# Performance work log

Measured on AMD Instinct MI355X. Metric: run time of the kernel, lower is better.

The kernel has to match this reference:

```python
import jax, jax.numpy as jnp
import numpy as np

B, S, DIM = 1, 2048, 4096
N_HEADS, N_KV_HEADS, HEAD_DIM = 32, 8, 128
REPEATS = N_HEADS // N_KV_HEADS
SLIDING_WINDOW = 2048
ROPE_THETA = 10000.0
NEG_INF = -1e9


def _rope_freqs(seqlen, head_dim):
    inv_freq = 1.0 / (ROPE_THETA ** (np.arange(0, head_dim, 2, dtype=np.float32) / head_dim))
    angles = np.arange(seqlen, dtype=np.float32)[:, None] * inv_freq[None, :]  # (S, D/2)
    return jnp.asarray(np.cos(angles)), jnp.asarray(np.sin(angles))


def _sliding_window_mask(seqlen, window):
    i = np.arange(seqlen)[:, None]
    j = np.arange(seqlen)[None, :]
    ok = (j <= i) & (i - j < window)
    return jnp.asarray(np.where(ok, 0.0, NEG_INF).astype(np.float32))


def setup_inputs() -> dict:
    key = jax.random.key(0)
    ks = jax.random.split(key, 5)
    x = jax.random.normal(ks[0], (B, S, DIM), dtype=jnp.float32)
    wq = jax.random.normal(ks[1], (N_HEADS * HEAD_DIM, DIM), dtype=jnp.float32) * 0.02
    wk = jax.random.normal(ks[2], (N_KV_HEADS * HEAD_DIM, DIM), dtype=jnp.float32) * 0.02
    wv = jax.random.normal(ks[3], (N_KV_HEADS * HEAD_DIM, DIM), dtype=jnp.float32) * 0.02
    wo = jax.random.normal(ks[4], (N_HEADS * HEAD_DIM, DIM), dtype=jnp.float32).T * 0.02
    wo = jnp.asarray(wo)  # (DIM, N_HEADS*HEAD_DIM), torch Linear weight layout (out,in)
    freqs_cos, freqs_sin = _rope_freqs(S, HEAD_DIM)
    mask = _sliding_window_mask(S, SLIDING_WINDOW)
    positions = jnp.arange(S, dtype=jnp.int64 if jax.config.jax_enable_x64 else jnp.int32)
    return {"x": x, "freqs_cos": freqs_cos, "freqs_sin": freqs_sin, "mask": mask,
            "positions": positions, "wq": wq, "wk": wk, "wv": wv, "wo": wo}


def _apply_rope(t, cos, sin):
    # t: (B, S, H, D); cos/sin: (S, D/2) broadcast as (1, S, 1, D/2)
    tr = t.reshape(*t.shape[:-1], -1, 2)
    re, im = tr[..., 0], tr[..., 1]
    c = cos[None, :, None, :]
    s = sin[None, :, None, :]
    out_re = re * c - im * s
    out_im = re * s + im * c
    return jnp.stack([out_re, out_im], axis=-1).reshape(t.shape)


def reference(x, freqs_cos, freqs_sin, mask, positions, wq, wk, wv, wo):
    bsz, seqlen, _ = x.shape
    xq = (x @ wq.T).reshape(bsz, seqlen, N_HEADS, HEAD_DIM)
    xk = (x @ wk.T).reshape(bsz, seqlen, N_KV_HEADS, HEAD_DIM)
    xv = (x @ wv.T).reshape(bsz, seqlen, N_KV_HEADS, HEAD_DIM)
    xq = _apply_rope(xq, freqs_cos, freqs_sin)
    xk = _apply_rope(xk, freqs_cos, freqs_sin)
    # prefill path (positions.shape[0] > 1): GQA repeat of current K/V
    key = jnp.repeat(xk, REPEATS, axis=2)   # (B, S, N_HEADS, D)
    value = jnp.repeat(xv, REPEATS, axis=2)
    scale = HEAD_DIM ** (-0.5)
    scores = jnp.einsum('bqhd,bkhd->bhqk', xq, key) * scale
    scores = scores + mask[None, None, :, :]
    probs = jax.nn.softmax(scores.astype(jnp.float32), axis=-1).astype(xq.dtype)
    out = jnp.einsum('bhqk,bkhd->bqhd', probs, value)
    out = out.reshape(bsz, seqlen, N_HEADS * HEAD_DIM)
    return out @ wo.T
```

## Files before the change

kernel.cpp:

```cpp
#include <hip/hip_runtime.h>

typedef __attribute__((ext_vector_type(4))) float f32x4;
typedef __attribute__((ext_vector_type(16))) float f32x16;
typedef __attribute__((ext_vector_type(8))) short bf16x8;
typedef __attribute__((ext_vector_type(4))) unsigned short u16x4;
typedef __attribute__((ext_vector_type(2))) unsigned short u16x2;
typedef __attribute__((ext_vector_type(4))) unsigned int u32x4;

#define SEQ 2048
#define DMODEL 4096

__device__ __forceinline__ unsigned short f2bf(float f) {
  unsigned int u = __float_as_uint(f);
  u += 0x7FFFu + ((u >> 16) & 1u);
  return (unsigned short)(u >> 16);
}

__device__ __forceinline__ void gload_lds16(const unsigned short* g, unsigned short* l) {
  __builtin_amdgcn_global_load_lds(
      (const __attribute__((address_space(1))) unsigned int*)g,
      (__attribute__((address_space(3))) unsigned int*)l, 16, 0, 0);
}

__device__ __forceinline__ unsigned int cvt_pk_bf16(float lo, float hi) {
  unsigned int r;
  asm("v_cvt_pk_bf16_f32 %0, %1, %2" : "=v"(r) : "v"(lo), "v"(hi));
  return r;
}

__global__ __launch_bounds__(256) void cvt_bf16(const float* __restrict__ in,
                                                unsigned short* __restrict__ out, int n4) {
  int i = blockIdx.x * 256 + threadIdx.x;
  if (i >= n4) return;
  f32x4 v = *(const f32x4*)(in + (size_t)i * 4);
  u16x4 o;
  o[0] = f2bf(v[0]); o[1] = f2bf(v[1]); o[2] = f2bf(v[2]); o[3] = f2bf(v[3]);
  *(u16x4*)(out + (size_t)i * 4) = o;
}

__global__ __launch_bounds__(256) void gemm_bt(const unsigned short* __restrict__ A,
                                               const unsigned short* __restrict__ B,
                                               float* __restrict__ C, int N) {
  __shared__ unsigned short As[128 * 64];
  __shared__ unsigned short Bs[128 * 64];
  const int K = 4096;
  const int bm = blockIdx.x, bn = blockIdx.y;
  const int t = threadIdx.x;
  const int lane = t & 63, w = t >> 6;
  const int wm = w >> 1, wn = w & 1;
  const int g = lane >> 4, q = lane & 15;

  const int srow = t >> 3;
  const int slb = (t & 7) ^ (srow & 7);
  const unsigned short* gA = A + (size_t)(bm * 128 + srow) * K + slb * 8;
  const unsigned short* gB = B + (size_t)(bn * 128 + srow) * K + slb * 8;
  unsigned short* lA = As + t * 8;
  unsigned short* lB = Bs + t * 8;

  f32x4 acc[4][4];
  for (int i = 0; i < 4; ++i)
    for (int j = 0; j < 4; ++j)
      for (int r = 0; r < 4; ++r) acc[i][j][r] = 0.f;

  for (int k0 = 0; k0 < K; k0 += 64) {
#pragma unroll
    for (int i = 0; i < 4; ++i) {
      gload_lds16(gA + (size_t)i * 32 * K + k0, lA + i * 2048);
      gload_lds16(gB + (size_t)i * 32 * K + k0, lB + i * 2048);
    }
    __syncthreads();
#pragma unroll
    for (int kk = 0; kk < 2; ++kk) {
      bf16x8 af[4], bfr[4];
#pragma unroll
      for (int i = 0; i < 4; ++i) {
        const int ra = wm * 64 + i * 16 + q;
        af[i] = *(const bf16x8*)&As[ra * 64 + (((kk * 4 + g) ^ (ra & 7)) * 8)];
        const int rb = wn * 64 + i * 16 + q;
        bfr[i] = *(const bf16x8*)&Bs[rb * 64 + (((kk * 4 + g) ^ (rb & 7)) * 8)];
      }
#pragma unroll
      for (int i = 0; i < 4; ++i)
#pragma unroll
        for (int j = 0; j < 4; ++j)
          acc[i][j] = __builtin_amdgcn_mfma_f32_16x16x32_bf16(af[i], bfr[j], acc[i][j], 0, 0, 0);
    }
    __syncthreads();
  }

  const int crow0 = bm * 128 + wm * 64 + g * 4;
  const int ccol0 = bn * 128 + wn * 64 + q;
#pragma unroll
  for (int i = 0; i < 4; ++i)
#pragma unroll
    for (int j = 0; j < 4; ++j) {
      float* cp = C + (size_t)(crow0 + i * 16) * N + ccol0 + j * 16;
#pragma unroll
      for (int r = 0; r < 4; ++r) cp[(size_t)r * N] = acc[i][j][r];
    }
}

__global__ __launch_bounds__(256) void rope_relayout(const float* __restrict__ X,
                                                     const float* __restrict__ cosT,
                                                     const float* __restrict__ sinT,
                                                     unsigned short* __restrict__ out,
                                                     int nheads, int ld) {
  int idx = blockIdx.x * 256 + threadIdx.x;
  int m = idx & 63;
  int h = (idx >> 6) % nheads;
  int s = idx / (nheads * 64);
  if (s >= SEQ) return;
  const float* xp = X + (size_t)s * ld + h * 128 + 2 * m;
  float re = xp[0], im = xp[1];
  float c = cosT[s * 64 + m], sn = sinT[s * 64 + m];
  u16x2 o;
  o[0] = f2bf(re * c - im * sn);
  o[1] = f2bf(re * sn + im * c);
  *(u16x2*)(out + ((size_t)h * SEQ + s) * 128 + 2 * m) = o;
}

__global__ __launch_bounds__(256) void v_transpose(const float* __restrict__ Vf,
                                                   unsigned short* __restrict__ VT) {
  __shared__ float tile[32][33];
  int s0 = blockIdx.x * 32, d0 = blockIdx.y * 32;
  int tx = threadIdx.x & 31, ty = threadIdx.x >> 5;
  for (int i = ty; i < 32; i += 8)
    tile[i][tx] = Vf[(size_t)(s0 + i) * 1024 + d0 + tx];
  __syncthreads();
  for (int i = ty; i < 32; i += 8)
    VT[(size_t)(d0 + i) * SEQ + s0 + tx] = f2bf(tile[tx][i]);
}

__global__ __launch_bounds__(256, 2) void attn_kernel(const unsigned short* __restrict__ Qh,
                                                      const unsigned short* __restrict__ Kh,
                                                      const unsigned short* __restrict__ VT,
                                                      unsigned short* __restrict__ Out) {
  const int x = blockIdx.x;
  const int h = (x & 7) * 4 + ((x >> 3) & 3);
  const int chunk = 15 - (x >> 5);
  const int kvh = h >> 2;
  const int t = threadIdx.x, w = t >> 6, lane = t & 63;
  const int ln = lane & 31, hi = lane >> 5;
  const int q0 = chunk * 128 + w * 32;

  const unsigned short* Qp = Qh + ((size_t)h * SEQ + q0 + ln) * 128 + hi * 8;
  const unsigned short* Kp = Kh + ((size_t)kvh * SEQ + ln) * 128 + hi * 8;
  const unsigned short* Vp = VT + ((size_t)(kvh * 128 + ln)) * SEQ + hi * 8;

  bf16x8 qf[8];
#pragma unroll
  for (int ds = 0; ds < 8; ++ds) qf[ds] = *(const bf16x8*)(Qp + ds * 16);

  f32x16 acc[4];
#pragma unroll
  for (int dt = 0; dt < 4; ++dt)
#pragma unroll
    for (int r = 0; r < 16; ++r) acc[dt][r] = 0.f;

  float m_run = -1e30f, l_run = 0.f;
  const float SCL = 0.08838834764831845f * 1.44269504088896f;

  for (int k0 = 0; k0 <= q0; k0 += 32) {
    bf16x8 vf[4][2];
#pragma unroll
    for (int dt = 0; dt < 4; ++dt)
#pragma unroll
      for (int ks = 0; ks < 2; ++ks)
        vf[dt][ks] = *(const bf16x8*)(Vp + (size_t)dt * 32 * SEQ + k0 + ks * 16);

    bf16x8 kf[8];
    const unsigned short* kp = Kp + (size_t)k0 * 128;
#pragma unroll
    for (int ds = 0; ds < 8; ++ds) kf[ds] = *(const bf16x8*)(kp + ds * 16);
    f32x16 s0, s1;
#pragma unroll
    for (int r = 0; r < 16; ++r) { s0[r] = 0.f; s1[r] = 0.f; }
#pragma unroll
    for (int ds = 0; ds < 4; ++ds) {
      s0 = __builtin_amdgcn_mfma_f32_32x32x16_bf16(kf[ds], qf[ds], s0, 0, 0, 0);
      s1 = __builtin_amdgcn_mfma_f32_32x32x16_bf16(kf[ds + 4], qf[ds + 4], s1, 0, 0, 0);
    }

    float sv[16];
#pragma unroll
    for (int r = 0; r < 16; ++r) {
      int kg = k0 + (r & 3) + 8 * (r >> 2) + 4 * hi;
      float vv = s0[r] + s1[r];
      sv[r] = (kg <= q0 + ln) ? vv : -1e30f;
    }
    float mx01 = fmaxf(sv[0], sv[1]), mx23 = fmaxf(sv[2], sv[3]);
    float mx45 = fmaxf(sv[4], sv[5]), mx67 = fmaxf(sv[6], sv[7]);
    float mx89 = fmaxf(sv[8], sv[9]), mxab = fmaxf(sv[10], sv[11]);
    float mxcd = fmaxf(sv[12], sv[13]), mxef = fmaxf(sv[14], sv[15]);
    float pm = fmaxf(fmaxf(fmaxf(mx01, mx23), fmaxf(mx45, mx67)),
                     fmaxf(fmaxf(mx89, mxab), fmaxf(mxcd, mxef)));
    pm = fmaxf(pm, __shfl_xor(pm, 32, 64));

    if (__any((pm - m_run) * SCL > 8.f)) {
      float m_new = fmaxf(m_run, pm);
      float corr = exp2f((m_run - m_new) * SCL);
      l_run *= corr;
#pragma unroll
      for (int r = 0; r < 16; ++r) {
        float cf = __shfl(corr, (r & 3) + 8 * (r >> 2) + 4 * hi, 64);
        acc[0][r] *= cf; acc[1][r] *= cf; acc[2][r] *= cf; acc[3][r] *= cf;
      }
      m_run = m_new;
    }

    float pv[16];
#pragma unroll
    for (int r = 0; r < 16; ++r) pv[r] = exp2f((sv[r] - m_run) * SCL);
    float a0 = (pv[0] + pv[1]) + (pv[2] + pv[3]);
    float a1 = (pv[4] + pv[5]) + (pv[6] + pv[7]);
    float a2 = (pv[8] + pv[9]) + (pv[10] + pv[11]);
    float a3 = (pv[12] + pv[13]) + (pv[14] + pv[15]);
    float ps = (a0 + a1) + (a2 + a3);
    ps += __shfl_xor(ps, 32, 64);
    l_run += ps;

    bf16x8 pa[2];
#pragma unroll
    for (int ks = 0; ks < 2; ++ks) {
      unsigned int X0 = cvt_pk_bf16(pv[8 * ks + 0], pv[8 * ks + 1]);
      unsigned int X1 = cvt_pk_bf16(pv[8 * ks + 2], pv[8 * ks + 3]);
      unsigned int Y0 = cvt_pk_bf16(pv[8 * ks + 4], pv[8 * ks + 5]);
      unsigned int Y1 = cvt_pk_bf16(pv[8 * ks + 6], pv[8 * ks + 7]);
      unsigned int sX0 = (unsigned int)__shfl_xor((int)X0, 32, 64);
      unsigned int sX1 = (unsigned int)__shfl_xor((int)X1, 32, 64);
      unsigned int sY0 = (unsigned int)__shfl_xor((int)Y0, 32, 64);
      unsigned int sY1 = (unsigned int)__shfl_xor((int)Y1, 32, 64);
      u32x4 pw;
      pw[0] = hi ? sY0 : X0;
      pw[1] = hi ? sY1 : X1;
      pw[2] = hi ? Y0 : sX0;
      pw[3] = hi ? Y1 : sX1;
      pa[ks] = __builtin_bit_cast(bf16x8, pw);
    }

#pragma unroll
    for (int dt = 0; dt < 4; ++dt) {
      acc[dt] = __builtin_amdgcn_mfma_f32_32x32x16_bf16(pa[0], vf[dt][0], acc[dt], 0, 0, 0);
      acc[dt] = __builtin_amdgcn_mfma_f32_32x32x16_bf16(pa[1], vf[dt][1], acc[dt], 0, 0, 0);
    }
  }

  float inv = 1.0f / l_run;
#pragma unroll
  for (int r = 0; r < 16; ++r) {
    float il = __shfl(inv, (r & 3) + 8 * (r >> 2) + 4 * hi, 64);
    int qg = q0 + (r & 3) + 8 * (r >> 2) + 4 * hi;
    unsigned short* op = Out + (size_t)qg * DMODEL + h * 128 + ln;
#pragma unroll
    for (int dt = 0; dt < 4; ++dt) op[dt * 32] = f2bf(acc[dt][r] * il);
  }
}

extern "C" void kernel_launch(void* const* d_in, const int* in_sizes, int n_in,
                              void* d_out, int out_size, void* d_ws, size_t ws_size,
                              hipStream_t stream) {
  (void)in_sizes; (void)n_in; (void)out_size; (void)ws_size;
  const float* x  = (const float*)d_in[0];
  const float* fc = (const float*)d_in[1];
  const float* fs = (const float*)d_in[2];
  const float* wq = (const float*)d_in[5];
  const float* wk = (const float*)d_in[6];
  const float* wv = (const float*)d_in[7];
  const float* wo = (const float*)d_in[8];
  float* out = (float*)d_out;

  char* ws = (char*)d_ws;
  const size_t MB = 1ull << 20;
  unsigned short* xb    = (unsigned short*)(ws + 0);
  unsigned short* wqb   = (unsigned short*)(ws + 16 * MB);
  unsigned short* wkb   = (unsigned short*)(ws + 48 * MB);
  unsigned short* wvb   = (unsigned short*)(ws + 56 * MB);
  float*          Qf    = (float*)(ws + 64 * MB);
  float*          Kf    = (float*)(ws + 96 * MB);
  float*          Vf    = (float*)(ws + 104 * MB);
  unsigned short* Qhb   = (unsigned short*)(ws + 112 * MB);
  unsigned short* Khb   = (unsigned short*)(ws + 128 * MB);
  unsigned short* VTb   = (unsigned short*)(ws + 132 * MB);
  unsigned short* attnb = (unsigned short*)(ws + 64 * MB);
  unsigned short* wob   = (unsigned short*)(ws + 16 * MB);

  cvt_bf16<<<8192, 256, 0, stream>>>(x, xb, 8388608 / 4);
  cvt_bf16<<<16384, 256, 0, stream>>>(wq, wqb, 16777216 / 4);
  cvt_bf16<<<4096, 256, 0, stream>>>(wk, wkb, 4194304 / 4);
  cvt_bf16<<<4096, 256, 0, stream>>>(wv, wvb, 4194304 / 4);

  gemm_bt<<<dim3(16, 32), 256, 0, stream>>>(xb, wqb, Qf, 4096);
  gemm_bt<<<dim3(16, 8), 256, 0, stream>>>(xb, wkb, Kf, 1024);
  gemm_bt<<<dim3(16, 8), 256, 0, stream>>>(xb, wvb, Vf, 1024);

  cvt_bf16<<<16384, 256, 0, stream>>>(wo, wob, 16777216 / 4);

  rope_relayout<<<16384, 256, 0, stream>>>(Qf, fc, fs, Qhb, 32, 4096);
  rope_relayout<<<4096, 256, 0, stream>>>(Kf, fc, fs, Khb, 8, 1024);
  v_transpose<<<dim3(64, 32), 256, 0, stream>>>(Vf, VTb);

  attn_kernel<<<512, 256, 0, stream>>>(Qhb, Khb, VTb, attnb);

  gemm_bt<<<dim3(16, 32), 256, 0, stream>>>(attnb, wob, out, 4096);
}
```

Before: 689.2 us.

## Balance causal attention work with paired tiles and split-K merge; fuse small launches

The attention kernel now pairs a short and a long causal query tile (p and 63-p) in each 128-thread block. The two waves split the key range of each tile and merge their partial softmax states through shared memory. This evens out per-block work and doubles the block count, so the causal triangle's load imbalance and tail shrink. It also merges the four fp32-to-bf16 conversions into one launch and the K and V projection GEMMs into one launch to cut launch overhead and raise occupancy. The cost is extra LDS traffic, barriers and a rescaling merge step per tile.

```diff
diff --git a/kernel.cpp b/kernel.cpp
--- a/kernel.cpp
+++ b/kernel.cpp
@@ -26,6 +26,24 @@
   unsigned int r;
   asm("v_cvt_pk_bf16_f32 %0, %1, %2" : "=v"(r) : "v"(lo), "v"(hi));
   return r;
+}
+
+__global__ __launch_bounds__(256) void cvt_bf16_multi(
+    const float* __restrict__ s0, unsigned short* __restrict__ d0, int n0,
+    const float* __restrict__ s1, unsigned short* __restrict__ d1, int n1,
+    const float* __restrict__ s2, unsigned short* __restrict__ d2, int n2,
+    const float* __restrict__ s3, unsigned short* __restrict__ d3, int n3) {
+  int i = blockIdx.x * 256 + threadIdx.x;
+  const float* s; unsigned short* d; int j = i;
+  if (j < n0) { s = s0; d = d0; }
+  else if ((j -= n0) < n1) { s = s1; d = d1; }
+  else if ((j -= n1) < n2) { s = s2; d = d2; }
+  else if ((j -= n2) < n3) { s = s3; d = d3; }
+  else return;
+  f32x4 v = *(const f32x4*)(s + (size_t)j * 4);
+  u16x4 o;
+  o[0] = f2bf(v[0]); o[1] = f2bf(v[1]); o[2] = f2bf(v[2]); o[3] = f2bf(v[3]);
+  *(u16x4*)(d + (size_t)j * 4) = o;
 }
 
 __global__ __launch_bounds__(256) void cvt_bf16(const float* __restrict__ in,
@@ -38,13 +56,13 @@
   *(u16x4*)(out + (size_t)i * 4) = o;
 }
 
-__global__ __launch_bounds__(256) void gemm_bt(const unsigned short* __restrict__ A,
-                                               const unsigned short* __restrict__ B,
-                                               float* __restrict__ C, int N) {
+__device__ __forceinline__ void gemm_bt_body(const unsigned short* __restrict__ A,
+                                             const unsigned short* __restrict__ B,
+                                             float* __restrict__ C, int N,
+                                             int bm, int bn) {
   __shared__ unsigned short As[128 * 64];
   __shared__ unsigned short Bs[128 * 64];
   const int K = 4096;
-  const int bm = blockIdx.x, bn = blockIdx.y;
   const int t = threadIdx.x;
   const int lane = t & 63, w = t >> 6;
   const int wm = w >> 1, wn = w & 1;
@@ -98,6 +116,22 @@
 #pragma unroll
       for (int r = 0; r < 4; ++r) cp[(size_t)r * N] = acc[i][j][r];
     }
+}
+
+__global__ __launch_bounds__(256) void gemm_bt(const unsigned short* __restrict__ A,
+                                               const unsigned short* __restrict__ B,
+                                               float* __restrict__ C, int N) {
+  gemm_bt_body(A, B, C, N, blockIdx.x, blockIdx.y);
+}
+
+__global__ __launch_bounds__(256) void gemm_bt_kv(const unsigned short* __restrict__ A,
+                                                  const unsigned short* __restrict__ BK,
+                                                  const unsigned short* __restrict__ BV,
+                                                  float* __restrict__ CK,
+                                                  float* __restrict__ CV) {
+  const int bn = blockIdx.y;
+  if (bn < 8) gemm_bt_body(A, BK, CK, 1024, blockIdx.x, bn);
+  else        gemm_bt_body(A, BV, CV, 1024, blockIdx.x, bn - 8);
 }
 
 __global__ __launch_bounds__(256) void rope_relayout(const float* __restrict__ X,
@@ -131,128 +165,171 @@
     VT[(size_t)(d0 + i) * SEQ + s0 + tx] = f2bf(tile[tx][i]);
 }
 
-__global__ __launch_bounds__(256, 2) void attn_kernel(const unsigned short* __restrict__ Qh,
+__global__ __launch_bounds__(128, 4) void attn_kernel(const unsigned short* __restrict__ Qh,
                                                       const unsigned short* __restrict__ Kh,
                                                       const unsigned short* __restrict__ VT,
                                                       unsigned short* __restrict__ Out) {
-  const int x = blockIdx.x;
-  const int h = (x & 7) * 4 + ((x >> 3) & 3);
-  const int chunk = 15 - (x >> 5);
+  __shared__ float mbuf[2][32];
+  __shared__ float lbuf[2][32];
+  __shared__ float abuf[64 * 64];
+
+  const int b = blockIdx.x;
+  const int h = (b & 7) * 4 + ((b >> 3) & 3);
+  const int p = b >> 5;
   const int kvh = h >> 2;
   const int t = threadIdx.x, w = t >> 6, lane = t & 63;
   const int ln = lane & 31, hi = lane >> 5;
-  const int q0 = chunk * 128 + w * 32;
-
-  const unsigned short* Qp = Qh + ((size_t)h * SEQ + q0 + ln) * 128 + hi * 8;
+
   const unsigned short* Kp = Kh + ((size_t)kvh * SEQ + ln) * 128 + hi * 8;
   const unsigned short* Vp = VT + ((size_t)(kvh * 128 + ln)) * SEQ + hi * 8;
-
-  bf16x8 qf[8];
-#pragma unroll
-  for (int ds = 0; ds < 8; ++ds) qf[ds] = *(const bf16x8*)(Qp + ds * 16);
-
-  f32x16 acc[4];
-#pragma unroll
-  for (int dt = 0; dt < 4; ++dt)
-#pragma unroll
-    for (int r = 0; r < 16; ++r) acc[dt][r] = 0.f;
-
-  float m_run = -1e30f, l_run = 0.f;
   const float SCL = 0.08838834764831845f * 1.44269504088896f;
 
-  for (int k0 = 0; k0 <= q0; k0 += 32) {
-    bf16x8 vf[4][2];
+  const int nA = p + 1, nB = 64 - p;
+  const int loA = (nA + 1) >> 1, loB = (nB + 1) >> 1;
+
+  for (int s = 0; s < 2; ++s) {
+    const int tile = (s == 0) ? p : 63 - p;
+    const int q0 = tile * 32;
+    int kbeg, kend;
+    if (s == 0) { kbeg = w ? loA : 0;  kend = w ? nA : loA; }
+    else        { kbeg = w ? 0 : loB;  kend = w ? loB : nB; }
+
+    const unsigned short* Qp = Qh + ((size_t)h * SEQ + q0 + ln) * 128 + hi * 8;
+    bf16x8 qf[8];
+#pragma unroll
+    for (int ds = 0; ds < 8; ++ds) qf[ds] = *(const bf16x8*)(Qp + ds * 16);
+
+    f32x16 acc[4];
 #pragma unroll
     for (int dt = 0; dt < 4; ++dt)
 #pragma unroll
-      for (int ks = 0; ks < 2; ++ks)
-        vf[dt][ks] = *(const bf16x8*)(Vp + (size_t)dt * 32 * SEQ + k0 + ks * 16);
-
-    bf16x8 kf[8];
-    const unsigned short* kp = Kp + (size_t)k0 * 128;
-#pragma unroll
-    for (int ds = 0; ds < 8; ++ds) kf[ds] = *(const bf16x8*)(kp + ds * 16);
-    f32x16 s0, s1;
-#pragma unroll
-    for (int r = 0; r < 16; ++r) { s0[r] = 0.f; s1[r] = 0.f; }
-#pragma unroll
-    for (int ds = 0; ds < 4; ++ds) {
-      s0 = __builtin_amdgcn_mfma_f32_32x32x16_bf16(kf[ds], qf[ds], s0, 0, 0, 0);
-      s1 = __builtin_amdgcn_mfma_f32_32x32x16_bf16(kf[ds + 4], qf[ds + 4], s1, 0, 0, 0);
-    }
-
-    float sv[16];
-#pragma unroll
-    for (int r = 0; r < 16; ++r) {
-      int kg = k0 + (r & 3) + 8 * (r >> 2) + 4 * hi;
-      float vv = s0[r] + s1[r];
-      sv[r] = (kg <= q0 + ln) ? vv : -1e30f;
-    }
-    float mx01 = fmaxf(sv[0], sv[1]), mx23 = fmaxf(sv[2], sv[3]);
-    float mx45 = fmaxf(sv[4], sv[5]), mx67 = fmaxf(sv[6], sv[7]);
-    float mx89 = fmaxf(sv[8], sv[9]), mxab = fmaxf(sv[10], sv[11]);
-    float mxcd = fmaxf(sv[12], sv[13]), mxef = fmaxf(sv[14], sv[15]);
-    float pm = fmaxf(fmaxf(fmaxf(mx01, mx23), fmaxf(mx45, mx67)),
-                     fmaxf(fmaxf(mx89, mxab), fmaxf(mxcd, mxef)));
-    pm = fmaxf(pm, __shfl_xor(pm, 32, 64));
-
-    if (__any((pm - m_run) * SCL > 8.f)) {
-      float m_new = fmaxf(m_run, pm);
-      float corr = exp2f((m_run - m_new) * SCL);
-      l_run *= corr;
+      for (int r = 0; r < 16; ++r) acc[dt][r] = 0.f;
+    float m_run = -1e30f, l_run = 0.f;
+
+    for (int kc = kbeg; kc < kend; ++kc) {
+      const int k0 = kc * 32;
+      bf16x8 vf[4][2];
+#pragma unroll
+      for (int dt = 0; dt < 4; ++dt)
+#pragma unroll
+        for (int ks = 0; ks < 2; ++ks)
+          vf[dt][ks] = *(const bf16x8*)(Vp + (size_t)dt * 32 * SEQ + k0 + ks * 16);
+
+      bf16x8 kf[8];
+      const unsigned short* kp = Kp + (size_t)k0 * 128;
+#pragma unroll
+      for (int ds = 0; ds < 8; ++ds) kf[ds] = *(const bf16x8*)(kp + ds * 16);
+      f32x16 s0v, s1v;
+#pragma unroll
+      for (int r = 0; r < 16; ++r) { s0v[r] = 0.f; s1v[r] = 0.f; }
+#pragma unroll
+      for (int ds = 0; ds < 4; ++ds) {
+        s0v = __builtin_amdgcn_mfma_f32_32x32x16_bf16(kf[ds], qf[ds], s0v, 0, 0, 0);
+        s1v = __builtin_amdgcn_mfma_f32_32x32x16_bf16(kf[ds + 4], qf[ds + 4], s1v, 0, 0, 0);
+      }
+
+      float sv[16];
 #pragma unroll
       for (int r = 0; r < 16; ++r) {
-        float cf = __shfl(corr, (r & 3) + 8 * (r >> 2) + 4 * hi, 64);
-        acc[0][r] *= cf; acc[1][r] *= cf; acc[2][r] *= cf; acc[3][r] *= cf;
-      }
-      m_run = m_new;
-    }
-
-    float pv[16];
-#pragma unroll
-    for (int r = 0; r < 16; ++r) pv[r] = exp2f((sv[r] - m_run) * SCL);
-    float a0 = (pv[0] + pv[1]) + (pv[2] + pv[3]);
-    float a1 = (pv[4] + pv[5]) + (pv[6] + pv[7]);
-    float a2 = (pv[8] + pv[9]) + (pv[10] + pv[11]);
-    float a3 = (pv[12] + pv[13]) + (pv[14] + pv[15]);
-    float ps = (a0 + a1) + (a2 + a3);
-    ps += __shfl_xor(ps, 32, 64);
-    l_run += ps;
-
-    bf16x8 pa[2];
-#pragma unroll
-    for (int ks = 0; ks < 2; ++ks) {
-      unsigned int X0 = cvt_pk_bf16(pv[8 * ks + 0], pv[8 * ks + 1]);
-      unsigned int X1 = cvt_pk_bf16(pv[8 * ks + 2], pv[8 * ks + 3]);
-      unsigned int Y0 = cvt_pk_bf16(pv[8 * ks + 4], pv[8 * ks + 5]);
-      unsigned int Y1 = cvt_pk_bf16(pv[8 * ks + 6], pv[8 * ks + 7]);
-      unsigned int sX0 = (unsigned int)__shfl_xor((int)X0, 32, 64);
-      unsigned int sX1 = (unsigned int)__shfl_xor((int)X1, 32, 64);
-      unsigned int sY0 = (unsigned int)__shfl_xor((int)Y0, 32, 64);
-      unsigned int sY1 = (unsigned int)__shfl_xor((int)Y1, 32, 64);
-      u32x4 pw;
-      pw[0] = hi ? sY0 : X0;
-      pw[1] = hi ? sY1 : X1;
-      pw[2] = hi ? Y0 : sX0;
-      pw[3] = hi ? Y1 : sX1;
-      pa[ks] = __builtin_bit_cast(bf16x8, pw);
-    }
-
-#pragma unroll
-    for (int dt = 0; dt < 4; ++dt) {
-      acc[dt] = __builtin_amdgcn_mfma_f32_32x32x16_bf16(pa[0], vf[dt][0], acc[dt], 0, 0, 0);
-      acc[dt] = __builtin_amdgcn_mfma_f32_32x32x16_bf16(pa[1], vf[dt][1], acc[dt], 0, 0, 0);
-    }
-  }
-
-  float inv = 1.0f / l_run;
-#pragma unroll
-  for (int r = 0; r < 16; ++r) {
-    float il = __shfl(inv, (r & 3) + 8 * (r >> 2) + 4 * hi, 64);
-    int qg = q0 + (r & 3) + 8 * (r >> 2) + 4 * hi;
-    unsigned short* op = Out + (size_t)qg * DMODEL + h * 128 + ln;
-#pragma unroll
-    for (int dt = 0; dt < 4; ++dt) op[dt * 32] = f2bf(acc[dt][r] * il);
+        int kg = k0 + (r & 3) + 8 * (r >> 2) + 4 * hi;
+        float vv = s0v[r] + s1v[r];
+        sv[r] = (kg <= q0 + ln) ? vv : -1e30f;
+      }
+      float mx01 = fmaxf(sv[0], sv[1]), mx23 = fmaxf(sv[2], sv[3]);
+      float mx45 = fmaxf(sv[4], sv[5]), mx67 = fmaxf(sv[6], sv[7]);
+      float mx89 = fmaxf(sv[8], sv[9]), mxab = fmaxf(sv[10], sv[11]);
+      float mxcd = fmaxf(sv[12], sv[13]), mxef = fmaxf(sv[14], sv[15]);
+      float pm = fmaxf(fmaxf(fmaxf(mx01, mx23), fmaxf(mx45, mx67)),
+                       fmaxf(fmaxf(mx89, mxab), fmaxf(mxcd, mxef)));
+      pm = fmaxf(pm, __shfl_xor(pm, 32, 64));
+
+      if (__any((pm - m_run) * SCL > 8.f)) {
+        float m_new = fmaxf(m_run, pm);
+        float corr = exp2f((m_run - m_new) * SCL);
+        l_run *= corr;
+#pragma unroll
+        for (int r = 0; r < 16; ++r) {
+          float cf = __shfl(corr, (r & 3) + 8 * (r >> 2) + 4 * hi, 64);
+          acc[0][r] *= cf; acc[1][r] *= cf; acc[2][r] *= cf; acc[3][r] *= cf;
+        }
+        m_run = m_new;
+      }
+
+      float pv[16];
+#pragma unroll
+      for (int r = 0; r < 16; ++r) pv[r] = exp2f((sv[r] - m_run) * SCL);
+      float a0 = (pv[0] + pv[1]) + (pv[2] + pv[3]);
+      float a1 = (pv[4] + pv[5]) + (pv[6] + pv[7]);
+      float a2 = (pv[8] + pv[9]) + (pv[10] + pv[11]);
+      float a3 = (pv[12] + pv[13]) + (pv[14] + pv[15]);
+      float ps = (a0 + a1) + (a2 + a3);
+      ps += __shfl_xor(ps, 32, 64);
+      l_run += ps;
+
+      bf16x8 pa[2];
+#pragma unroll
+      for (int ks = 0; ks < 2; ++ks) {
+        unsigned int X0 = cvt_pk_bf16(pv[8 * ks + 0], pv[8 * ks + 1]);
+        unsigned int X1 = cvt_pk_bf16(pv[8 * ks + 2], pv[8 * ks + 3]);
+        unsigned int Y0 = cvt_pk_bf16(pv[8 * ks + 4], pv[8 * ks + 5]);
+        unsigned int Y1 = cvt_pk_bf16(pv[8 * ks + 6], pv[8 * ks + 7]);
+        unsigned int sX0 = (unsigned int)__shfl_xor((int)X0, 32, 64);
+        unsigned int sX1 = (unsigned int)__shfl_xor((int)X1, 32, 64);
+        unsigned int sY0 = (unsigned int)__shfl_xor((int)Y0, 32, 64);
+        unsigned int sY1 = (unsigned int)__shfl_xor((int)Y1, 32, 64);
+        u32x4 pw;
+        pw[0] = hi ? sY0 : X0;
+        pw[1] = hi ? sY1 : X1;
+        pw[2] = hi ? Y0 : sX0;
+        pw[3] = hi ? Y1 : sX1;
+        pa[ks] = __builtin_bit_cast(bf16x8, pw);
+      }
+
+#pragma unroll
+      for (int dt = 0; dt < 4; ++dt) {
+        acc[dt] = __builtin_amdgcn_mfma_f32_32x32x16_bf16(pa[0], vf[dt][0], acc[dt], 0, 0, 0);
+        acc[dt] = __builtin_amdgcn_mfma_f32_32x32x16_bf16(pa[1], vf[dt][1], acc[dt], 0, 0, 0);
+      }
+    }
+
+    if (hi == 0) { mbuf[w][ln] = m_run; lbuf[w][ln] = l_run; }
+    __syncthreads();
+
+    const int wW = (s == 0) ? 1 : 0;
+    if (w == wW) {
+#pragma unroll
+      for (int r = 0; r < 16; ++r) {
+        const int row = (r & 3) + 8 * (r >> 2) + 4 * hi;
+        float m0 = mbuf[0][row], m1 = mbuf[1][row];
+        float ms = fmaxf(m0, m1);
+        float fown = exp2f(((w ? m1 : m0) - ms) * SCL);
+#pragma unroll
+        for (int dt = 0; dt < 4; ++dt)
+          abuf[(dt * 16 + r) * 64 + lane] = acc[dt][r] * fown;
+      }
+    }
+    __syncthreads();
+    if (w != wW) {
+#pragma unroll
+      for (int r = 0; r < 16; ++r) {
+        const int row = (r & 3) + 8 * (r >> 2) + 4 * hi;
+        float m0 = mbuf[0][row], m1 = mbuf[1][row];
+        float ms = fmaxf(m0, m1);
+        float f0 = exp2f((m0 - ms) * SCL);
+        float f1 = exp2f((m1 - ms) * SCL);
+        float ls = lbuf[0][row] * f0 + lbuf[1][row] * f1;
+        float inv = 1.0f / ls;
+        float fown = w ? f1 : f0;
+        const int qg = q0 + row;
+        unsigned short* op = Out + (size_t)qg * DMODEL + h * 128 + ln;
+#pragma unroll
+        for (int dt = 0; dt < 4; ++dt) {
+          float val = (acc[dt][r] * fown + abuf[(dt * 16 + r) * 64 + lane]) * inv;
+          op[dt * 32] = f2bf(val);
+        }
+      }
+    }
+    __syncthreads();
   }
 }
 
@@ -284,14 +361,13 @@
   unsigned short* attnb = (unsigned short*)(ws + 64 * MB);
   unsigned short* wob   = (unsigned short*)(ws + 16 * MB);
 
-  cvt_bf16<<<8192, 256, 0, stream>>>(x, xb, 8388608 / 4);
-  cvt_bf16<<<16384, 256, 0, stream>>>(wq, wqb, 16777216 / 4);
-  cvt_bf16<<<4096, 256, 0, stream>>>(wk, wkb, 4194304 / 4);
-  cvt_bf16<<<4096, 256, 0, stream>>>(wv, wvb, 4194304 / 4);
+  cvt_bf16_multi<<<32768, 256, 0, stream>>>(x, xb, 2097152,
+                                            wq, wqb, 4194304,
+                                            wk, wkb, 1048576,
+                                            wv, wvb, 1048576);
 
   gemm_bt<<<dim3(16, 32), 256, 0, stream>>>(xb, wqb, Qf, 4096);
-  gemm_bt<<<dim3(16, 8), 256, 0, stream>>>(xb, wkb, Kf, 1024);
-  gemm_bt<<<dim3(16, 8), 256, 0, stream>>>(xb, wvb, Vf, 1024);
+  gemm_bt_kv<<<dim3(16, 16), 256, 0, stream>>>(xb, wkb, wvb, Kf, Vf);
 
   cvt_bf16<<<16384, 256, 0, stream>>>(wo, wob, 16777216 / 4);
 
@@ -299,7 +375,7 @@
   rope_relayout<<<4096, 256, 0, stream>>>(Kf, fc, fs, Khb, 8, 1024);
   v_transpose<<<dim3(64, 32), 256, 0, stream>>>(Vf, VTb);
 
-  attn_kernel<<<512, 256, 0, stream>>>(Qhb, Khb, VTb, attnb);
+  attn_kernel<<<1024, 128, 0, stream>>>(Qhb, Khb, VTb, attnb);
 
   gemm_bt<<<dim3(16, 32), 256, 0, stream>>>(attnb, wob, out, 4096);
 }
```

After: 749.4 us. 8.7% more time.
